# Performance work log

Hardware: AMD Instinct MI355X
Metric: run time of the kernel (lower is better)

## Reference

```python
import jax, jax.numpy as jnp
import numpy as np

NUM_HEADS = 8
D_MODEL = 512
D_Q = D_MODEL // NUM_HEADS
B, S = 4, 2048


def setup_inputs() -> dict:
    key = jax.random.key(0)
    ks = jax.random.split(key, 7)
    bound = 1.0 / np.sqrt(D_MODEL)  # kaiming_uniform with a=sqrt(5) on fan_in=d_model
    return {
        "x_query": jax.random.normal(ks[0], (B, S, D_MODEL), dtype=jnp.float32),
        "x_key": jax.random.normal(ks[1], (B, S, D_MODEL), dtype=jnp.float32),
        "x_value": jax.random.normal(ks[2], (B, S, D_MODEL), dtype=jnp.float32),
        "Q": jax.random.uniform(ks[3], (NUM_HEADS, D_MODEL, D_Q), minval=-bound, maxval=bound, dtype=jnp.float32),
        "K": jax.random.uniform(ks[4], (NUM_HEADS, D_MODEL, D_Q), minval=-bound, maxval=bound, dtype=jnp.float32),
        "V": jax.random.uniform(ks[5], (NUM_HEADS, D_MODEL, D_Q), minval=-bound, maxval=bound, dtype=jnp.float32),
        "Wout": jax.random.uniform(ks[6], (D_MODEL, D_MODEL), minval=-bound, maxval=bound, dtype=jnp.float32),
    }


def reference(x_query, x_key, x_value, Q, K, V, Wout):
    # per-head projections: [B,S,d_model] x [H,d_model,d_q] -> [B,H,S,d_q]
    q = jnp.einsum('bsd,hdq->bhsq', x_query, Q)
    k = jnp.einsum('bsd,hdq->bhsq', x_key, K)
    v = jnp.einsum('bsd,hdq->bhsq', x_value, V)
    scale = 1.0 / jnp.sqrt(jnp.asarray(q.shape[-1], q.dtype))
    scores = jnp.einsum('bhsq,bhtq->bhst', q, k) * scale  # [B,H,S,S]
    attn = jax.nn.softmax(scores, axis=-1)
    heads = jnp.einsum('bhst,bhtq->bhsq', attn, v)  # [B,H,S,d_q]
    # faithful to original: .view(B, S, -1) on [B,H,S,d_q] layout (no transpose)
    concat = heads.reshape(heads.shape[0], heads.shape[2], -1)
    return concat @ Wout.T
```

## Files before the change

### kernel.cpp

```cpp
#include <hip/hip_runtime.h>
#include <math.h>

#define BATCH 4
#define SEQ   2048
#define DM    512
#define NH    8
#define DQ    64
#define BS    (BATCH*SEQ)
#define BPAD  72

typedef short  short8  __attribute__((ext_vector_type(8)));
typedef float  floatx4 __attribute__((ext_vector_type(4)));
typedef unsigned short ushort8 __attribute__((ext_vector_type(8)));

__device__ __forceinline__ unsigned short f2bf(float f) {
    unsigned u = __float_as_uint(f);
    unsigned r = (u + 0x7fffu + ((u >> 16) & 1u)) >> 16;
    return (unsigned short)r;
}

__device__ __forceinline__ void async_copy16(const void* g, void* l) {
    __builtin_amdgcn_global_load_lds(
        (const __attribute__((address_space(1))) unsigned int*)g,
        (__attribute__((address_space(3))) unsigned int*)l, 16, 0, 0);
}

__global__ __launch_bounds__(256) void convert_x_kernel(
    const float* __restrict__ xq, const float* __restrict__ xk,
    const float* __restrict__ xv, unsigned short* __restrict__ xb)
{
    const float* X = (blockIdx.y == 0) ? xq : (blockIdx.y == 1) ? xk : xv;
    unsigned short* O = xb + (size_t)blockIdx.y * (BS * DM);
    const int i = (blockIdx.x * 256 + threadIdx.x) * 4;
    float4 v = *(const float4*)(X + i);
    ushort4 o;
    o.x = f2bf(v.x); o.y = f2bf(v.y); o.z = f2bf(v.z); o.w = f2bf(v.w);
    *(ushort4*)(O + i) = o;
}

__global__ __launch_bounds__(256) void convert_w_kernel(
    const float* __restrict__ Wq, const float* __restrict__ Wk,
    const float* __restrict__ Wv, const float* __restrict__ Wo,
    unsigned short* __restrict__ wt, unsigned short* __restrict__ wo)
{
    const int which = blockIdx.y;
    const int idx = blockIdx.x * 256 + threadIdx.x;
    if (which == 3) {
        float4 v = *(const float4*)(Wo + (size_t)idx * 4);
        ushort4 o;
        o.x = f2bf(v.x); o.y = f2bf(v.y); o.z = f2bf(v.z); o.w = f2bf(v.w);
        *(ushort4*)(wo + (size_t)idx * 4) = o;
    } else {
        const float* W = (which == 0) ? Wq : (which == 1) ? Wk : Wv;
        const int n   = idx >> 7;
        const int dd0 = (idx & 127) * 4;
        const int h = n >> 6, d = n & 63;
        ushort4 o;
        o.x = f2bf(W[((size_t)h * DM + dd0 + 0) * DQ + d]);
        o.y = f2bf(W[((size_t)h * DM + dd0 + 1) * DQ + d]);
        o.z = f2bf(W[((size_t)h * DM + dd0 + 2) * DQ + d]);
        o.w = f2bf(W[((size_t)h * DM + dd0 + 3) * DQ + d]);
        *(ushort4*)(wt + (size_t)which * (DM * DM) + (size_t)n * DM + dd0) = o;
    }
}

__global__ __launch_bounds__(256) void qkv_gemm_kernel(
    const unsigned short* __restrict__ xb, const unsigned short* __restrict__ wt,
    unsigned short* __restrict__ Oq, unsigned short* __restrict__ Ok,
    unsigned short* __restrict__ Ovt)
{
    __shared__ unsigned short As[128][64];
    __shared__ unsigned short Bs[128][64];

    const int which = blockIdx.z;
    const unsigned short* A  = xb + (size_t)which * (BS * DM);
    const unsigned short* Bt = wt + (size_t)which * (DM * DM);

    const int m0 = blockIdx.x * 128;
    const int n0 = blockIdx.y * 128;
    const int t = threadIdx.x, w = t >> 6, lane = t & 63;
    const int quad = lane >> 4, qr = lane & 15;
    const int lr = lane >> 3;
    const int lc = (lane & 7) * 8;
    const int mw = 64 * (w >> 1), nw = 64 * (w & 1);

    floatx4 acc[4][4] = {};

    for (int k0 = 0; k0 < DM; k0 += 64) {
        #pragma unroll
        for (int i = 0; i < 4; ++i) {
            const int row = i * 32 + w * 8;
            async_copy16(A  + (size_t)(m0 + row + lr) * DM + k0 + lc, &As[row][0]);
            async_copy16(Bt + (size_t)(n0 + row + lr) * DM + k0 + lc, &Bs[row][0]);
        }
        __syncthreads();
        #pragma unroll
        for (int kh = 0; kh < 2; ++kh) {
            short8 af[4], bf[4];
            #pragma unroll
            for (int si = 0; si < 4; ++si)
                af[si] = *(const short8*)&As[mw + 16 * si + qr][kh * 32 + quad * 8];
            #pragma unroll
            for (int sj = 0; sj < 4; ++sj)
                bf[sj] = *(const short8*)&Bs[nw + 16 * sj + qr][kh * 32 + quad * 8];
            #pragma unroll
            for (int si = 0; si < 4; ++si)
                #pragma unroll
                for (int sj = 0; sj < 4; ++sj)
                    acc[si][sj] = __builtin_amdgcn_mfma_f32_16x16x32_bf16(
                        af[si], bf[sj], acc[si][sj], 0, 0, 0);
        }
        __syncthreads();
    }

    const float osc = (which == 0) ? 0.125f : 1.0f;
    if (which < 2) {
        unsigned short* O = (which == 0) ? Oq : Ok;
        #pragma unroll
        for (int si = 0; si < 4; ++si) {
            #pragma unroll
            for (int sj = 0; sj < 4; ++sj) {
                const int col = n0 + nw + 16 * sj + qr;
                const int h = col >> 6, d = col & 63;
                #pragma unroll
                for (int r = 0; r < 4; ++r) {
                    const int row = m0 + mw + 16 * si + quad * 4 + r;
                    const int b = row >> 11, s = row & (SEQ - 1);
                    O[((size_t)(b * NH + h) * SEQ + s) * DQ + d] = f2bf(acc[si][sj][r] * osc);
                }
            }
        }
    } else {
        #pragma unroll
        for (int si = 0; si < 4; ++si) {
            #pragma unroll
            for (int sj = 0; sj < 4; ++sj) {
                const int col = n0 + nw + 16 * sj + qr;
                const int h = col >> 6, d = col & 63;
                #pragma unroll
                for (int r = 0; r < 4; ++r) {
                    const int row = m0 + mw + 16 * si + quad * 4 + r;
                    const int b = row >> 11, s = row & (SEQ - 1);
                    Ovt[((size_t)(b * NH + h) * DQ + d) * SEQ + s] = f2bf(acc[si][sj][r]);
                }
            }
        }
    }
}

__global__ __launch_bounds__(256) void out_gemm_kernel(
    const unsigned short* __restrict__ A, const unsigned short* __restrict__ Bt,
    float* __restrict__ C)
{
    __shared__ unsigned short As[128][64];
    __shared__ unsigned short Bs[128][64];

    const int m0 = blockIdx.x * 128;
    const int n0 = blockIdx.y * 128;
    const int t = threadIdx.x, w = t >> 6, lane = t & 63;
    const int quad = lane >> 4, qr = lane & 15;
    const int lr = lane >> 3;
    const int lc = (lane & 7) * 8;
    const int mw = 64 * (w >> 1), nw = 64 * (w & 1);

    floatx4 acc[4][4] = {};

    for (int k0 = 0; k0 < DM; k0 += 64) {
        #pragma unroll
        for (int i = 0; i < 4; ++i) {
            const int row = i * 32 + w * 8;
            async_copy16(A  + (size_t)(m0 + row + lr) * DM + k0 + lc, &As[row][0]);
            async_copy16(Bt + (size_t)(n0 + row + lr) * DM + k0 + lc, &Bs[row][0]);
        }
        __syncthreads();
        #pragma unroll
        for (int kh = 0; kh < 2; ++kh) {
            short8 af[4], bf[4];
            #pragma unroll
            for (int si = 0; si < 4; ++si)
                af[si] = *(const short8*)&As[mw + 16 * si + qr][kh * 32 + quad * 8];
            #pragma unroll
            for (int sj = 0; sj < 4; ++sj)
                bf[sj] = *(const short8*)&Bs[nw + 16 * sj + qr][kh * 32 + quad * 8];
            #pragma unroll
            for (int si = 0; si < 4; ++si)
                #pragma unroll
                for (int sj = 0; sj < 4; ++sj)
                    acc[si][sj] = __builtin_amdgcn_mfma_f32_16x16x32_bf16(
                        af[si], bf[sj], acc[si][sj], 0, 0, 0);
        }
        __syncthreads();
    }

    #pragma unroll
    for (int si = 0; si < 4; ++si) {
        #pragma unroll
        for (int sj = 0; sj < 4; ++sj) {
            const int col = n0 + nw + 16 * sj + qr;
            #pragma unroll
            for (int r = 0; r < 4; ++r) {
                const int row = m0 + mw + 16 * si + quad * 4 + r;
                C[(size_t)row * DM + col] = acc[si][sj][r];
            }
        }
    }
}

__global__ __launch_bounds__(256) void attn_kernel(
    const unsigned short* __restrict__ Qp, const unsigned short* __restrict__ Kp,
    const unsigned short* __restrict__ Vtp, unsigned short* __restrict__ Hd)
{
    __shared__ unsigned short Qs[64][BPAD];
    __shared__ unsigned short Ks[64][BPAD];
    __shared__ unsigned short Vts[64][BPAD];
    __shared__ unsigned short Ps[64][BPAD];

    const int s0 = blockIdx.x * 64;
    const int h  = blockIdx.y;
    const int b  = blockIdx.z;
    const size_t bh    = (size_t)(b * NH + h);
    const size_t base  = bh * SEQ * DQ;
    const size_t vbase = bh * DQ * SEQ;

    const int t    = threadIdx.x;
    const int w    = t >> 6;
    const int lane = t & 63;
    const int quad = lane >> 4;
    const int qr   = lane & 15;

    {
        const unsigned short* g = Qp + base + (size_t)s0 * DQ;
        #pragma unroll
        for (int i = 0; i < 2; ++i) {
            const int c = t + 256 * i;
            const int row = c >> 3, col8 = (c & 7) * 8;
            *(ushort8*)&Qs[row][col8] = *(const ushort8*)(g + row * DQ + col8);
        }
    }
    __syncthreads();
    const short8 aq0 = *(const short8*)&Qs[16 * w + qr][quad * 8];
    const short8 aq1 = *(const short8*)&Qs[16 * w + qr][quad * 8 + 32];

    floatx4 acc_o[4] = {};
    float l_lane = 0.f;

    ushort8 kreg[2], vreg[2];
    {
        const unsigned short* gk = Kp + base;
        const unsigned short* gv = Vtp + vbase;
        #pragma unroll
        for (int i = 0; i < 2; ++i) {
            const int c = t + 256 * i;
            const int row = c >> 3, col8 = (c & 7) * 8;
            kreg[i] = *(const ushort8*)(gk + row * DQ + col8);
            vreg[i] = *(const ushort8*)(gv + (size_t)row * SEQ + col8);
        }
    }

    for (int kt = 0; kt < SEQ; kt += 64) {
        __syncthreads();
        #pragma unroll
        for (int i = 0; i < 2; ++i) {
            const int c = t + 256 * i;
            const int row = c >> 3, col8 = (c & 7) * 8;
            *(ushort8*)&Ks[row][col8]  = kreg[i];
            *(ushort8*)&Vts[row][col8] = vreg[i];
        }
        __syncthreads();

        if (kt + 64 < SEQ) {
            const unsigned short* gk = Kp + base + (size_t)(kt + 64) * DQ;
            const unsigned short* gv = Vtp + vbase + (kt + 64);
            #pragma unroll
            for (int i = 0; i < 2; ++i) {
                const int c = t + 256 * i;
                const int row = c >> 3, col8 = (c & 7) * 8;
                kreg[i] = *(const ushort8*)(gk + row * DQ + col8);
                vreg[i] = *(const ushort8*)(gv + (size_t)row * SEQ + col8);
            }
        }

        #pragma unroll
        for (int si = 0; si < 4; ++si) {
            const short8 ak0 = *(const short8*)&Ks[16 * si + qr][quad * 8];
            const short8 ak1 = *(const short8*)&Ks[16 * si + qr][quad * 8 + 32];
            floatx4 z = {0.f, 0.f, 0.f, 0.f};
            z = __builtin_amdgcn_mfma_f32_16x16x32_bf16(ak0, aq0, z, 0, 0, 0);
            z = __builtin_amdgcn_mfma_f32_16x16x32_bf16(ak1, aq1, z, 0, 0, 0);
            const float p0 = __expf(z[0]), p1 = __expf(z[1]);
            const float p2 = __expf(z[2]), p3 = __expf(z[3]);
            l_lane += (p0 + p1) + (p2 + p3);
            ushort4 pk;
            pk.x = f2bf(p0); pk.y = f2bf(p1); pk.z = f2bf(p2); pk.w = f2bf(p3);
            *(ushort4*)&Ps[16 * w + qr][16 * si + quad * 4] = pk;
        }

        const short8 ap0 = *(const short8*)&Ps[16 * w + qr][quad * 8];
        const short8 ap1 = *(const short8*)&Ps[16 * w + qr][quad * 8 + 32];
        #pragma unroll
        for (int c = 0; c < 4; ++c) {
            const short8 bv0 = *(const short8*)&Vts[16 * c + qr][quad * 8];
            const short8 bv1 = *(const short8*)&Vts[16 * c + qr][quad * 8 + 32];
            acc_o[c] = __builtin_amdgcn_mfma_f32_16x16x32_bf16(ap0, bv0, acc_o[c], 0, 0, 0);
            acc_o[c] = __builtin_amdgcn_mfma_f32_16x16x32_bf16(ap1, bv1, acc_o[c], 0, 0, 0);
        }
    }

    l_lane += __shfl_xor(l_lane, 16);
    l_lane += __shfl_xor(l_lane, 32);
    float inv_l[4];
    #pragma unroll
    for (int r = 0; r < 4; ++r)
        inv_l[r] = 1.0f / __shfl(l_lane, quad * 4 + r);

    #pragma unroll
    for (int c = 0; c < 4; ++c)
        #pragma unroll
        for (int r = 0; r < 4; ++r)
            Hd[base + (size_t)(s0 + 16 * w + quad * 4 + r) * DQ + 16 * c + qr] =
                f2bf(acc_o[c][r] * inv_l[r]);
}

extern "C" void kernel_launch(void* const* d_in, const int* in_sizes, int n_in,
                              void* d_out, int out_size, void* d_ws, size_t ws_size,
                              hipStream_t stream) {
    const float* xq = (const float*)d_in[0];
    const float* xk = (const float*)d_in[1];
    const float* xv = (const float*)d_in[2];
    const float* Qw = (const float*)d_in[3];
    const float* Kw = (const float*)d_in[4];
    const float* Vw = (const float*)d_in[5];
    const float* Wo = (const float*)d_in[6];
    float* out = (float*)d_out;

    unsigned short* ws = (unsigned short*)d_ws;
    unsigned short* xb    = ws;
    unsigned short* wt    = ws + (size_t)12582912;
    unsigned short* wo    = ws + (size_t)13369344;
    unsigned short* q_ws  = ws + (size_t)13631488;
    unsigned short* k_ws  = ws + (size_t)17825792;
    unsigned short* vt_ws = ws + (size_t)22020096;
    unsigned short* h_ws  = ws + (size_t)26214400;

    convert_x_kernel<<<dim3(4096, 3), 256, 0, stream>>>(xq, xk, xv, xb);
    convert_w_kernel<<<dim3(256, 4), 256, 0, stream>>>(Qw, Kw, Vw, Wo, wt, wo);
    qkv_gemm_kernel<<<dim3(64, 4, 3), 256, 0, stream>>>(xb, wt, q_ws, k_ws, vt_ws);
    attn_kernel<<<dim3(SEQ / 64, NH, BATCH), 256, 0, stream>>>(q_ws, k_ws, vt_ws, h_ws);
    out_gemm_kernel<<<dim3(64, 4), 256, 0, stream>>>(h_ws, wo, out);
}
```

Measured before the change: 213.1 us.

## Fuse input bf16 conversion into QKV GEMM, widen attention query tile, use exp2

Drops the separate fp32-to-bf16 conversion kernel for the activations. The QKV GEMM now loads fp32 inputs directly, converts them in registers and stores bf16 into padded shared memory. Each attention block now covers 128 query rows, two 16-row tiles per wave, so every K/V tile loaded into shared memory is reused twice. The softmax uses exp2 with log2(e) folded into the Q scale. The trade-off is synchronous A loads in the GEMM instead of async copies, higher register pressure, and half as many attention blocks.

Measured after the change: 214.7 us. No clear change (+0.8%).

```diff
diff --git a/kernel.cpp b/kernel.cpp
--- a/kernel.cpp
+++ b/kernel.cpp
@@ -8,6 +8,9 @@
 #define DQ    64
 #define BS    (BATCH*SEQ)
 #define BPAD  72
+#define APAD  72
+
+#define QSCALE 0.18033688011112042f
 
 typedef short  short8  __attribute__((ext_vector_type(8)));
 typedef float  floatx4 __attribute__((ext_vector_type(4)));
@@ -23,19 +26,6 @@
     __builtin_amdgcn_global_load_lds(
         (const __attribute__((address_space(1))) unsigned int*)g,
         (__attribute__((address_space(3))) unsigned int*)l, 16, 0, 0);
-}
-
-__global__ __launch_bounds__(256) void convert_x_kernel(
-    const float* __restrict__ xq, const float* __restrict__ xk,
-    const float* __restrict__ xv, unsigned short* __restrict__ xb)
-{
-    const float* X = (blockIdx.y == 0) ? xq : (blockIdx.y == 1) ? xk : xv;
-    unsigned short* O = xb + (size_t)blockIdx.y * (BS * DM);
-    const int i = (blockIdx.x * 256 + threadIdx.x) * 4;
-    float4 v = *(const float4*)(X + i);
-    ushort4 o;
-    o.x = f2bf(v.x); o.y = f2bf(v.y); o.z = f2bf(v.z); o.w = f2bf(v.w);
-    *(ushort4*)(O + i) = o;
 }
 
 __global__ __launch_bounds__(256) void convert_w_kernel(
@@ -65,15 +55,16 @@
 }
 
 __global__ __launch_bounds__(256) void qkv_gemm_kernel(
-    const unsigned short* __restrict__ xb, const unsigned short* __restrict__ wt,
+    const float* __restrict__ Xq, const float* __restrict__ Xk,
+    const float* __restrict__ Xv, const unsigned short* __restrict__ wt,
     unsigned short* __restrict__ Oq, unsigned short* __restrict__ Ok,
     unsigned short* __restrict__ Ovt)
 {
-    __shared__ unsigned short As[128][64];
+    __shared__ unsigned short As[128][APAD];
     __shared__ unsigned short Bs[128][64];
 
     const int which = blockIdx.z;
-    const unsigned short* A  = xb + (size_t)which * (BS * DM);
+    const float* X = (which == 0) ? Xq : (which == 1) ? Xk : Xv;
     const unsigned short* Bt = wt + (size_t)which * (DM * DM);
 
     const int m0 = blockIdx.x * 128;
@@ -82,6 +73,8 @@
     const int quad = lane >> 4, qr = lane & 15;
     const int lr = lane >> 3;
     const int lc = (lane & 7) * 8;
+    const int arow = t >> 4;
+    const int acol = (t & 15) * 4;
     const int mw = 64 * (w >> 1), nw = 64 * (w & 1);
 
     floatx4 acc[4][4] = {};
@@ -90,8 +83,15 @@
         #pragma unroll
         for (int i = 0; i < 4; ++i) {
             const int row = i * 32 + w * 8;
-            async_copy16(A  + (size_t)(m0 + row + lr) * DM + k0 + lc, &As[row][0]);
             async_copy16(Bt + (size_t)(n0 + row + lr) * DM + k0 + lc, &Bs[row][0]);
+        }
+        #pragma unroll
+        for (int i = 0; i < 8; ++i) {
+            const int row = i * 16 + arow;
+            float4 x4 = *(const float4*)(X + (size_t)(m0 + row) * DM + k0 + acol);
+            ushort4 o;
+            o.x = f2bf(x4.x); o.y = f2bf(x4.y); o.z = f2bf(x4.z); o.w = f2bf(x4.w);
+            *(ushort4*)&As[row][acol] = o;
         }
         __syncthreads();
         #pragma unroll
@@ -113,7 +113,7 @@
         __syncthreads();
     }
 
-    const float osc = (which == 0) ? 0.125f : 1.0f;
+    const float osc = (which == 0) ? QSCALE : 1.0f;
     if (which < 2) {
         unsigned short* O = (which == 0) ? Oq : Ok;
         #pragma unroll
@@ -210,12 +210,12 @@
     const unsigned short* __restrict__ Qp, const unsigned short* __restrict__ Kp,
     const unsigned short* __restrict__ Vtp, unsigned short* __restrict__ Hd)
 {
-    __shared__ unsigned short Qs[64][BPAD];
+    __shared__ unsigned short Qs[128][BPAD];
     __shared__ unsigned short Ks[64][BPAD];
     __shared__ unsigned short Vts[64][BPAD];
-    __shared__ unsigned short Ps[64][BPAD];
-
-    const int s0 = blockIdx.x * 64;
+    __shared__ unsigned short Ps[128][BPAD];
+
+    const int s0 = blockIdx.x * 128;
     const int h  = blockIdx.y;
     const int b  = blockIdx.z;
     const size_t bh    = (size_t)(b * NH + h);
@@ -231,18 +231,22 @@
     {
         const unsigned short* g = Qp + base + (size_t)s0 * DQ;
         #pragma unroll
-        for (int i = 0; i < 2; ++i) {
+        for (int i = 0; i < 4; ++i) {
             const int c = t + 256 * i;
             const int row = c >> 3, col8 = (c & 7) * 8;
             *(ushort8*)&Qs[row][col8] = *(const ushort8*)(g + row * DQ + col8);
         }
     }
     __syncthreads();
-    const short8 aq0 = *(const short8*)&Qs[16 * w + qr][quad * 8];
-    const short8 aq1 = *(const short8*)&Qs[16 * w + qr][quad * 8 + 32];
-
-    floatx4 acc_o[4] = {};
-    float l_lane = 0.f;
+    short8 aq[2][2];
+    #pragma unroll
+    for (int tq = 0; tq < 2; ++tq) {
+        aq[tq][0] = *(const short8*)&Qs[32 * w + 16 * tq + qr][quad * 8];
+        aq[tq][1] = *(const short8*)&Qs[32 * w + 16 * tq + qr][quad * 8 + 32];
+    }
+
+    floatx4 acc_o[2][4] = {};
+    float l_lane[2] = {0.f, 0.f};
 
     ushort8 kreg[2], vreg[2];
     {
@@ -284,41 +288,56 @@
         for (int si = 0; si < 4; ++si) {
             const short8 ak0 = *(const short8*)&Ks[16 * si + qr][quad * 8];
             const short8 ak1 = *(const short8*)&Ks[16 * si + qr][quad * 8 + 32];
-            floatx4 z = {0.f, 0.f, 0.f, 0.f};
-            z = __builtin_amdgcn_mfma_f32_16x16x32_bf16(ak0, aq0, z, 0, 0, 0);
-            z = __builtin_amdgcn_mfma_f32_16x16x32_bf16(ak1, aq1, z, 0, 0, 0);
-            const float p0 = __expf(z[0]), p1 = __expf(z[1]);
-            const float p2 = __expf(z[2]), p3 = __expf(z[3]);
-            l_lane += (p0 + p1) + (p2 + p3);
-            ushort4 pk;
-            pk.x = f2bf(p0); pk.y = f2bf(p1); pk.z = f2bf(p2); pk.w = f2bf(p3);
-            *(ushort4*)&Ps[16 * w + qr][16 * si + quad * 4] = pk;
-        }
-
-        const short8 ap0 = *(const short8*)&Ps[16 * w + qr][quad * 8];
-        const short8 ap1 = *(const short8*)&Ps[16 * w + qr][quad * 8 + 32];
+            #pragma unroll
+            for (int tq = 0; tq < 2; ++tq) {
+                floatx4 z = {0.f, 0.f, 0.f, 0.f};
+                z = __builtin_amdgcn_mfma_f32_16x16x32_bf16(ak0, aq[tq][0], z, 0, 0, 0);
+                z = __builtin_amdgcn_mfma_f32_16x16x32_bf16(ak1, aq[tq][1], z, 0, 0, 0);
+                const float p0 = exp2f(z[0]), p1 = exp2f(z[1]);
+                const float p2 = exp2f(z[2]), p3 = exp2f(z[3]);
+                l_lane[tq] += (p0 + p1) + (p2 + p3);
+                ushort4 pk;
+                pk.x = f2bf(p0); pk.y = f2bf(p1); pk.z = f2bf(p2); pk.w = f2bf(p3);
+                *(ushort4*)&Ps[32 * w + 16 * tq + qr][16 * si + quad * 4] = pk;
+            }
+        }
+
+        short8 ap[2][2];
+        #pragma unroll
+        for (int tq = 0; tq < 2; ++tq) {
+            ap[tq][0] = *(const short8*)&Ps[32 * w + 16 * tq + qr][quad * 8];
+            ap[tq][1] = *(const short8*)&Ps[32 * w + 16 * tq + qr][quad * 8 + 32];
+        }
         #pragma unroll
         for (int c = 0; c < 4; ++c) {
             const short8 bv0 = *(const short8*)&Vts[16 * c + qr][quad * 8];
             const short8 bv1 = *(const short8*)&Vts[16 * c + qr][quad * 8 + 32];
-            acc_o[c] = __builtin_amdgcn_mfma_f32_16x16x32_bf16(ap0, bv0, acc_o[c], 0, 0, 0);
-            acc_o[c] = __builtin_amdgcn_mfma_f32_16x16x32_bf16(ap1, bv1, acc_o[c], 0, 0, 0);
-        }
-    }
-
-    l_lane += __shfl_xor(l_lane, 16);
-    l_lane += __shfl_xor(l_lane, 32);
-    float inv_l[4];
+            #pragma unroll
+            for (int tq = 0; tq < 2; ++tq) {
+                acc_o[tq][c] = __builtin_amdgcn_mfma_f32_16x16x32_bf16(
+                    ap[tq][0], bv0, acc_o[tq][c], 0, 0, 0);
+                acc_o[tq][c] = __builtin_amdgcn_mfma_f32_16x16x32_bf16(
+                    ap[tq][1], bv1, acc_o[tq][c], 0, 0, 0);
+            }
+        }
+    }
+
     #pragma unroll
-    for (int r = 0; r < 4; ++r)
-        inv_l[r] = 1.0f / __shfl(l_lane, quad * 4 + r);
-
-    #pragma unroll
-    for (int c = 0; c < 4; ++c)
+    for (int tq = 0; tq < 2; ++tq) {
+        float l = l_lane[tq];
+        l += __shfl_xor(l, 16);
+        l += __shfl_xor(l, 32);
+        float inv_l[4];
         #pragma unroll
         for (int r = 0; r < 4; ++r)
-            Hd[base + (size_t)(s0 + 16 * w + quad * 4 + r) * DQ + 16 * c + qr] =
-                f2bf(acc_o[c][r] * inv_l[r]);
+            inv_l[r] = 1.0f / __shfl(l, quad * 4 + r);
+        #pragma unroll
+        for (int c = 0; c < 4; ++c)
+            #pragma unroll
+            for (int r = 0; r < 4; ++r)
+                Hd[base + (size_t)(s0 + 32 * w + 16 * tq + quad * 4 + r) * DQ + 16 * c + qr] =
+                    f2bf(acc_o[tq][c][r] * inv_l[r]);
+    }
 }
 
 extern "C" void kernel_launch(void* const* d_in, const int* in_sizes, int n_in,
@@ -334,17 +353,15 @@
     float* out = (float*)d_out;
 
     unsigned short* ws = (unsigned short*)d_ws;
-    unsigned short* xb    = ws;
-    unsigned short* wt    = ws + (size_t)12582912;
-    unsigned short* wo    = ws + (size_t)13369344;
-    unsigned short* q_ws  = ws + (size_t)13631488;
-    unsigned short* k_ws  = ws + (size_t)17825792;
-    unsigned short* vt_ws = ws + (size_t)22020096;
-    unsigned short* h_ws  = ws + (size_t)26214400;
-
-    convert_x_kernel<<<dim3(4096, 3), 256, 0, stream>>>(xq, xk, xv, xb);
+    unsigned short* wt    = ws;
+    unsigned short* wo    = ws + (size_t)786432;
+    unsigned short* q_ws  = ws + (size_t)1048576;
+    unsigned short* k_ws  = ws + (size_t)5242880;
+    unsigned short* vt_ws = ws + (size_t)9437184;
+    unsigned short* h_ws  = ws + (size_t)13631488;
+
     convert_w_kernel<<<dim3(256, 4), 256, 0, stream>>>(Qw, Kw, Vw, Wo, wt, wo);
-    qkv_gemm_kernel<<<dim3(64, 4, 3), 256, 0, stream>>>(xb, wt, q_ws, k_ws, vt_ws);
-    attn_kernel<<<dim3(SEQ / 64, NH, BATCH), 256, 0, stream>>>(q_ws, k_ws, vt_ws, h_ws);
+    qkv_gemm_kernel<<<dim3(64, 4, 3), 256, 0, stream>>>(xq, xk, xv, wt, q_ws, k_ws, vt_ws);
+    attn_kernel<<<dim3(SEQ / 128, NH, BATCH), 256, 0, stream>>>(q_ws, k_ws, vt_ws, h_ws);
     out_gemm_kernel<<<dim3(64, 4), 256, 0, stream>>>(h_ws, wo, out);
 }
```
